# Performance work log

Measured on AMD Instinct MI355X. Metric: run time of the kernel, lower is better.

Reference implementation:

```python
import jax, jax.numpy as jnp
import numpy as np

B, S, H, NH = 4, 2048, 1024, 16
HD = H // NH
EPS = 1e-12


def setup_inputs() -> dict:
    key = jax.random.key(0)
    ks = jax.random.split(key, 12)
    sc = 0.02
    return {
        "query": jax.random.normal(ks[0], (B, S, H), dtype=jnp.float32),
        "attention_mask": jnp.zeros((B, 1, 1, S), dtype=jnp.float32),
        "Wq": jax.random.normal(ks[1], (H, H), dtype=jnp.float32) * sc,
        "bq": jnp.zeros((H,), dtype=jnp.float32),
        "Wk": jax.random.normal(ks[2], (H, H), dtype=jnp.float32) * sc,
        "bk": jnp.zeros((H,), dtype=jnp.float32),
        "Wv": jax.random.normal(ks[3], (H, H), dtype=jnp.float32) * sc,
        "bv": jnp.zeros((H,), dtype=jnp.float32),
        "Wd": jax.random.normal(ks[4], (H, H), dtype=jnp.float32) * sc,
        "bd": jnp.zeros((H,), dtype=jnp.float32),
        "ln_gamma": jnp.ones((H,), dtype=jnp.float32),
        "ln_beta": jnp.zeros((H,), dtype=jnp.float32),
    }


def reference(query, attention_mask, Wq, bq, Wk, bk, Wv, bv, Wd, bd, ln_gamma, ln_beta):
    # QKV projections: [B,S,H] -> [B,S,NH,HD]
    q = (query @ Wq + bq).reshape(B, S, NH, HD)
    k = (query @ Wk + bk).reshape(B, S, NH, HD)
    v = (query @ Wv + bv).reshape(B, S, NH, HD)
    # scores: [B,NH,S,S]
    scores = jnp.einsum("bqhd,bkhd->bhqk", q, k) / jnp.sqrt(jnp.float32(HD))
    scores = scores + attention_mask
    probs = jax.nn.softmax(scores, axis=-1)  # attn_dropout p=0 (eval)
    ctx = jnp.einsum("bhqk,bkhd->bqhd", probs, v).reshape(B, S, H)
    hidden = ctx @ Wd + bd  # out_dropout p=0 (eval)
    # pre-LN residual path: LN(hidden) + query
    mu = jnp.mean(hidden, axis=-1, keepdims=True)
    var = jnp.mean(jnp.square(hidden - mu), axis=-1, keepdims=True)
    hidden = (hidden - mu) * jax.lax.rsqrt(var + EPS) * ln_gamma + ln_beta
    return hidden + query
```

## Files before the change

### kernel.cpp

```cpp
#include <hip/hip_runtime.h>
#include <stdint.h>

#define Bn 4
#define Sn 2048
#define Hn 1024
#define NHn 16
#define Mn 8192

typedef unsigned short bf_t;
typedef __attribute__((ext_vector_type(8))) short s16x8;
typedef __attribute__((ext_vector_type(4))) short s16x4;
typedef __attribute__((ext_vector_type(8))) unsigned short u16x8;
typedef __attribute__((ext_vector_type(4))) unsigned short u16x4;
typedef __attribute__((ext_vector_type(4))) float f32x4;
typedef __attribute__((ext_vector_type(4))) unsigned int u32x4;
typedef __attribute__((ext_vector_type(2))) unsigned int u32x2;

__device__ __forceinline__ bf_t f2bf(float f) {
  unsigned int u = __float_as_uint(f);
  u += 0x7fffu + ((u >> 16) & 1u);
  return (bf_t)(u >> 16);
}

__device__ __forceinline__ unsigned pk2(float lo, float hi) {
  return __builtin_amdgcn_perm(__float_as_uint(hi), __float_as_uint(lo), 0x07060302u);
}
__device__ __forceinline__ s16x4 pack4(float a0, float a1, float a2, float a3) {
  u32x2 t;
  t[0] = pk2(a0, a1);
  t[1] = pk2(a2, a3);
  return __builtin_bit_cast(s16x4, t);
}

#define MFMA16K16(a, b, c) __builtin_amdgcn_mfma_f32_16x16x16bf16_1k(a, b, c, 0, 0, 0)
#define MFMA32(a, b, c) __builtin_amdgcn_mfma_f32_16x16x32_bf16(a, b, c, 0, 0, 0)

#define GLOAD16(gp, lp) __builtin_amdgcn_global_load_lds(              \
    (__attribute__((address_space(1))) void*)(gp),                     \
    (__attribute__((address_space(3))) void*)(lp), 16, 0, 0)

__global__ __launch_bounds__(256)
void prep(const float* __restrict__ Wq, const float* __restrict__ Wk,
          const float* __restrict__ Wv, const float* __restrict__ Wd,
          const float* __restrict__ query,
          bf_t* __restrict__ Wt, bf_t* __restrict__ Wdt, bf_t* __restrict__ Xb) {
  __shared__ float tile[32][33];
  const int z = blockIdx.z;
  const int tx = threadIdx.x;
  const int ty = threadIdx.y;
  if (z == 4) {
    const int bid = blockIdx.y * 32 + blockIdx.x;
    const int t = ty * 32 + tx;
    const size_t base = (size_t)bid * 8192 + t * 4;
#pragma unroll
    for (int i = 0; i < 8; i++) {
      const f32x4 v = *(const f32x4*)(query + base + i * 1024);
      u16x4 o;
      o[0] = f2bf(v[0]); o[1] = f2bf(v[1]); o[2] = f2bf(v[2]); o[3] = f2bf(v[3]);
      *(u16x4*)(Xb + base + i * 1024) = o;
    }
    return;
  }
  const float* W = (z == 0) ? Wq : (z == 1) ? Wk : (z == 2) ? Wv : Wd;
  bf_t* dst = (z < 3) ? Wt + (size_t)z * Hn * Hn : Wdt;
  const int n0 = blockIdx.x * 32, k0 = blockIdx.y * 32;
#pragma unroll
  for (int i = 0; i < 4; i++)
    tile[ty + i * 8][tx] = W[(size_t)(k0 + ty + i * 8) * Hn + n0 + tx];
  __syncthreads();
#pragma unroll
  for (int i = 0; i < 4; i++) {
    const int nn = ty + i * 8, kk = tx;
    dst[(size_t)(n0 + nn) * Hn + k0 + kk] = f2bf(tile[kk][nn]);
  }
}

__global__ __launch_bounds__(256, 3)
void gemm_bt(const bf_t* __restrict__ A, const bf_t* __restrict__ Bt,
             const float* __restrict__ b0, const float* __restrict__ b1,
             const float* __restrict__ b2, void* __restrict__ outp,
             int N, int K, int out_bf16)
{
  __shared__ bf_t As[2][4096];
  __shared__ bf_t Bs[2][4096];
  const int tid = threadIdx.x;
  const int wave = tid >> 6, lane = tid & 63;
  const int l15 = lane & 15, quad = lane >> 4;
  const int bm = blockIdx.y * 128, bn = blockIdx.x * 128;
  const int wm = (wave >> 1) * 64, wn = (wave & 1) * 64;
  const int srow = tid >> 2;
  const int scol = (tid & 3) * 8;

  const bf_t* Ag = A + (size_t)(bm + srow) * K + scol;
  const bf_t* Bg = Bt + (size_t)(bn + srow) * K + scol;

  f32x4 acc[4][4] = {};

  GLOAD16(Ag, As[0] + tid * 8);
  GLOAD16(Ag + (size_t)64 * K, As[0] + 2048 + tid * 8);
  GLOAD16(Bg, Bs[0] + tid * 8);
  GLOAD16(Bg + (size_t)64 * K, Bs[0] + 2048 + tid * 8);

  const int nIter = K >> 5;
  for (int i = 0; i < nIter; i++) {
    const int cur = i & 1;
    __syncthreads();
    if (i + 1 < nIter) {
      const int k0 = (i + 1) * 32;
      GLOAD16(Ag + k0, As[cur ^ 1] + tid * 8);
      GLOAD16(Ag + (size_t)64 * K + k0, As[cur ^ 1] + 2048 + tid * 8);
      GLOAD16(Bg + k0, Bs[cur ^ 1] + tid * 8);
      GLOAD16(Bg + (size_t)64 * K + k0, Bs[cur ^ 1] + 2048 + tid * 8);
    }
    s16x8 af[4], bfr[4];
#pragma unroll
    for (int mi = 0; mi < 4; mi++)
      af[mi] = *(const s16x8*)&As[cur][(wm + mi * 16 + l15) * 32 + quad * 8];
#pragma unroll
    for (int ni = 0; ni < 4; ni++)
      bfr[ni] = *(const s16x8*)&Bs[cur][(wn + ni * 16 + l15) * 32 + quad * 8];
#pragma unroll
    for (int mi = 0; mi < 4; mi++)
#pragma unroll
      for (int ni = 0; ni < 4; ni++)
        acc[mi][ni] = __builtin_amdgcn_mfma_f32_16x16x32_bf16(af[mi], bfr[ni], acc[mi][ni], 0, 0, 0);
  }

#pragma unroll
  for (int ni = 0; ni < 4; ni++) {
    const int gn = bn + wn + ni * 16 + l15;
    const float* bp = (gn < 1024) ? b0 : ((gn < 2048) ? b1 : b2);
    const float bias = bp[gn & 1023];
#pragma unroll
    for (int mi = 0; mi < 4; mi++) {
#pragma unroll
      for (int r = 0; r < 4; r++) {
        const int gm = bm + wm + mi * 16 + quad * 4 + r;
        const float v = acc[mi][ni][r] + bias;
        if (out_bf16) ((bf_t*)outp)[(size_t)gm * N + gn] = f2bf(v);
        else          ((float*)outp)[(size_t)gm * N + gn] = v;
      }
    }
  }
}

__global__ __launch_bounds__(256)
void kvswz(const bf_t* __restrict__ qkv, bf_t* __restrict__ Vf,
           const float* __restrict__ mask, bf_t* __restrict__ Fb) {
  __shared__ unsigned int P32[64 * 33];
  const int t = threadIdx.x;
  const int bh = blockIdx.y, b = bh >> 4, h = bh & 15;
  const int k0 = blockIdx.x * 64;

  {
    const int kp = t >> 3;
    const int d0 = (t & 7) * 8;
    const int kg = k0 + 2 * kp;
    const float f0 = __builtin_amdgcn_exp2f(mask[b * Sn + kg] * 1.44269504f);
    const float f1 = __builtin_amdgcn_exp2f(mask[b * Sn + kg + 1] * 1.44269504f);
    const bf_t* p0 = qkv + (size_t)(b * Sn + kg) * 3072 + 2048 + h * 64 + d0;
    const u16x8 r0 = *(const u16x8*)p0;
    const u16x8 r1 = *(const u16x8*)(p0 + 3072);
#pragma unroll
    for (int j = 0; j < 8; j++) {
      const float v0 = __uint_as_float((unsigned)r0[j] << 16) * f0;
      const float v1 = __uint_as_float((unsigned)r1[j] << 16) * f1;
      P32[(d0 + j) * 33 + kp] = pk2(v0, v1);
    }
  }
  if (h == 0 && t < 64) {
    const float fm = __builtin_amdgcn_exp2f(mask[b * Sn + k0 + t] * 1.44269504f);
    Fb[b * Sn + k0 + t] = f2bf(fm);
  }
  __syncthreads();
  bf_t* dst0 = Vf + ((size_t)(bh * 32 + blockIdx.x) * 8) * 512;
#pragma unroll
  for (int i = 0; i < 2; i++) {
    const int p = t + i * 256;
    const int fp = p >> 6, lane = p & 63;
    const int dvblk = fp >> 1, kpair = fp & 1;
    const int l15 = lane & 15, quad = (lane >> 4) & 3;
    const int d = dvblk * 16 + l15;
    const int c = kpair * 16 + quad * 2;
    u32x4 w;
    w[0] = P32[d * 33 + c];
    w[1] = P32[d * 33 + c + 1];
    w[2] = P32[d * 33 + c + 8];
    w[3] = P32[d * 33 + c + 9];
    *(u32x4*)(dst0 + (size_t)(kpair * 4 + dvblk) * 512 + lane * 8) = w;
  }
}

__global__ __launch_bounds__(512)
void attn(const bf_t* __restrict__ qkv, const bf_t* __restrict__ Vf,
          const bf_t* __restrict__ Fb, bf_t* __restrict__ ctx)
{
  __shared__ __align__(16) bf_t KV[2][2][2][2048];
  __shared__ __align__(16) bf_t Fs[2048];

  const int tid = threadIdx.x;
  const int wave = tid >> 6, lane = tid & 63;
  const int g = wave >> 2, wv = wave & 3;
  const int tg = tid & 255;
  const int l15 = lane & 15, quad = lane >> 4;
  const int idx = blockIdx.x;
  const int bh = idx & 63, b = bh >> 4, h = bh & 15;
  const int q0 = (idx >> 6) * 256;

  if (tid < 256) GLOAD16(Fb + (size_t)b * Sn + tid * 8, Fs + tid * 8);

  s16x8 aq[4][2];
#pragma unroll
  for (int qf = 0; qf < 4; qf++) {
    const bf_t* qp = qkv + (size_t)(b * Sn + q0 + wv * 64 + qf * 16 + l15) * 3072 + h * 64;
    aq[qf][0] = *(const s16x8*)(qp + quad * 8);
    aq[qf][1] = *(const s16x8*)(qp + 32 + quad * 8);
  }

  f32x4 lacc[4] = {};
  f32x4 o[4][4] = {};

  const int ks = tg >> 7, kh = (tg >> 6) & 1;
  const int lg = tg & 63, l15g = lg & 15, quadg = lg >> 4;
  const bf_t* kq = qkv + (size_t)(b * Sn + g * 1024 + ks * 16 + l15g) * 3072
                   + 1024 + h * 64 + kh * 32 + quadg * 8;
  const bf_t* vb = Vf + (size_t)bh * 131072 + (size_t)g * 65536;
  const float C1 = 0.125f * 1.44269504f;

  GLOAD16(kq, KV[g][0][0] + tg * 8);
  GLOAD16(vb + tg * 8, KV[g][1][0] + tg * 8);

  for (int it = 0; it < 32; ++it) {
    const int cur = it & 1;
    __syncthreads();
    if (it < 31) {
      GLOAD16(kq + (size_t)(it + 1) * 98304, KV[g][0][cur ^ 1] + tg * 8);
      GLOAD16(vb + (it + 1) * 2048 + tg * 8, KV[g][1][cur ^ 1] + tg * 8);
    }

    s16x4 pb[4][2];
#pragma unroll
    for (int e = 0; e < 2; e++) {
      const s16x8 k0f = *(const s16x8*)&KV[g][0][cur][(e * 2 + 0) * 512 + lane * 8];
      const s16x8 k1f = *(const s16x8*)&KV[g][0][cur][(e * 2 + 1) * 512 + lane * 8];
      const s16x4 ff = *(const s16x4*)&Fs[g * 1024 + it * 32 + e * 16 + quad * 4];
#pragma unroll
      for (int qf = 0; qf < 4; qf++) {
        f32x4 acc = {};
        __builtin_amdgcn_s_setprio(1);
        acc = MFMA32(k0f, aq[qf][0], acc);
        acc = MFMA32(k1f, aq[qf][1], acc);
        __builtin_amdgcn_s_setprio(0);
        const float p0 = __builtin_amdgcn_exp2f(acc[0] * C1);
        const float p1 = __builtin_amdgcn_exp2f(acc[1] * C1);
        const float p2 = __builtin_amdgcn_exp2f(acc[2] * C1);
        const float p3 = __builtin_amdgcn_exp2f(acc[3] * C1);
        pb[qf][e] = pack4(p0, p1, p2, p3);
        lacc[qf] = MFMA16K16(ff, pb[qf][e], lacc[qf]);
      }
    }

    __builtin_amdgcn_s_setprio(1);
#pragma unroll
    for (int dvblk = 0; dvblk < 4; dvblk++) {
      const s16x8 vv = *(const s16x8*)&KV[g][1][cur][dvblk * 512 + lane * 8];
      const s16x4 vlo = {vv[0], vv[1], vv[2], vv[3]};
      const s16x4 vhi = {vv[4], vv[5], vv[6], vv[7]};
#pragma unroll
      for (int qf = 0; qf < 4; qf++) {
        o[qf][dvblk] = MFMA16K16(vlo, pb[qf][0], o[qf][dvblk]);
        o[qf][dvblk] = MFMA16K16(vhi, pb[qf][1], o[qf][dvblk]);
      }
    }
    __builtin_amdgcn_s_setprio(0);
  }

  float* sm = (float*)&KV[0][0][0][0];
  float* sl = (float*)&Fs[0];
#pragma unroll
  for (int qh = 0; qh < 2; qh++) {
    __syncthreads();
    if (g == 1) {
#pragma unroll
      for (int lq = 0; lq < 2; lq++) {
        const int qf = qh * 2 + lq;
        const int rp = wv * 32 + lq * 16 + l15;
#pragma unroll
        for (int dvblk = 0; dvblk < 4; dvblk++) {
          const int col = (dvblk * 16 + quad * 4 + l15 * 4) & 63;
          *(f32x4*)&sm[rp * 64 + col] = o[qf][dvblk];
        }
        if (quad == 0) sl[rp] = lacc[qf][0];
      }
    }
    __syncthreads();
    if (g == 0) {
#pragma unroll
      for (int lq = 0; lq < 2; lq++) {
        const int qf = qh * 2 + lq;
        const int rp = wv * 32 + lq * 16 + l15;
        const float inv = 1.f / (lacc[qf][0] + sl[rp]);
        const size_t grow = (size_t)(b * Sn + q0 + wv * 64 + qf * 16 + l15);
#pragma unroll
        for (int dvblk = 0; dvblk < 4; dvblk++) {
          const int col = (dvblk * 16 + quad * 4 + l15 * 4) & 63;
          const f32x4 o2 = *(const f32x4*)&sm[rp * 64 + col];
          u16x4 ov;
#pragma unroll
          for (int r = 0; r < 4; r++) ov[r] = f2bf((o[qf][dvblk][r] + o2[r]) * inv);
          *(u16x4*)&ctx[grow * Hn + h * 64 + dvblk * 16 + quad * 4] = ov;
        }
      }
    }
  }
}

__global__ __launch_bounds__(256)
void ln_res(const float* __restrict__ hid, const float* __restrict__ query,
            const float* __restrict__ gamma, const float* __restrict__ beta,
            float* __restrict__ out)
{
  const int row = blockIdx.x, t = threadIdx.x;
  const f32x4 h = *(const f32x4*)(hid + (size_t)row * Hn + t * 4);
  float s = h[0] + h[1] + h[2] + h[3];
  float ss = h[0]*h[0] + h[1]*h[1] + h[2]*h[2] + h[3]*h[3];
#pragma unroll
  for (int m = 32; m; m >>= 1) { s += __shfl_xor(s, m); ss += __shfl_xor(ss, m); }
  __shared__ float red[8];
  if ((t & 63) == 0) { red[t >> 6] = s; red[4 + (t >> 6)] = ss; }
  __syncthreads();
  s = red[0] + red[1] + red[2] + red[3];
  ss = red[4] + red[5] + red[6] + red[7];
  const float mu = s * (1.f / Hn);
  const float rs = rsqrtf(ss * (1.f / Hn) - mu * mu + 1e-12f);
  const f32x4 q = *(const f32x4*)(query + (size_t)row * Hn + t * 4);
  const f32x4 g = *(const f32x4*)(gamma + t * 4);
  const f32x4 be = *(const f32x4*)(beta + t * 4);
  f32x4 o;
#pragma unroll
  for (int j = 0; j < 4; j++) o[j] = (h[j] - mu) * rs * g[j] + be[j] + q[j];
  *(f32x4*)(out + (size_t)row * Hn + t * 4) = o;
}

extern "C" void kernel_launch(void* const* d_in, const int* in_sizes, int n_in,
                              void* d_out, int out_size, void* d_ws, size_t ws_size,
                              hipStream_t stream) {
  const float* query = (const float*)d_in[0];
  const float* mask  = (const float*)d_in[1];
  const float* Wq = (const float*)d_in[2];
  const float* bq = (const float*)d_in[3];
  const float* Wk = (const float*)d_in[4];
  const float* bk = (const float*)d_in[5];
  const float* Wv = (const float*)d_in[6];
  const float* bv = (const float*)d_in[7];
  const float* Wd = (const float*)d_in[8];
  const float* bd = (const float*)d_in[9];
  const float* gamma = (const float*)d_in[10];
  const float* beta  = (const float*)d_in[11];

  char* w = (char*)d_ws;
  bf_t* Xb  = (bf_t*)w;  w += (size_t)Mn * Hn * 2;
  bf_t* Wt  = (bf_t*)w;  w += (size_t)3 * Hn * Hn * 2;
  bf_t* Wdt = (bf_t*)w;  w += (size_t)Hn * Hn * 2;
  bf_t* QKV = (bf_t*)w;  w += (size_t)Mn * 3 * Hn * 2;
  bf_t* Vf  = (bf_t*)w;  w += (size_t)64 * 32 * 4096 * 2;
  bf_t* Ctx = (bf_t*)w;  w += (size_t)Mn * Hn * 2;
  float* Hid = (float*)w;  w += (size_t)Mn * Hn * 4;
  bf_t* Fb = (bf_t*)w;

  prep<<<dim3(32, 32, 5), dim3(32, 8), 0, stream>>>(Wq, Wk, Wv, Wd, query, Wt, Wdt, Xb);
  gemm_bt<<<dim3(24, 64), 256, 0, stream>>>(Xb, Wt, bq, bk, bv, QKV, 3072, 1024, 1);
  kvswz<<<dim3(32, 64), 256, 0, stream>>>(QKV, Vf, mask, Fb);
  attn<<<512, 512, 0, stream>>>(QKV, Vf, Fb, Ctx);
  gemm_bt<<<dim3(8, 64), 256, 0, stream>>>(Ctx, Wdt, bd, bd, bd, Hid, 1024, 1024, 0);
  ln_res<<<Mn, 256, 0, stream>>>(Hid, query, gamma, beta, (float*)d_out);
}
```

Measured before the change: 357.0 us.

## Halve attention block size to 256 threads with 128 queries per block

The attention kernel now runs 1024 blocks of 256 threads, each covering 128 queries with 2 waves per key-split group instead of 4. Each thread issues twice as many K/V staging loads per iteration to fill the same shared tiles. The cross-group reduction epilogue collapses to a single pass, since the shared scratch now holds all rows. The intent is more blocks and better occupancy and tail balance across CUs, at the cost of loading each K/V tile for half as many queries.

```diff
diff --git a/kernel.cpp b/kernel.cpp
--- a/kernel.cpp
+++ b/kernel.cpp
@@ -191,7 +191,7 @@
   }
 }
 
-__global__ __launch_bounds__(512)
+__global__ __launch_bounds__(256)
 void attn(const bf_t* __restrict__ qkv, const bf_t* __restrict__ Vf,
           const bf_t* __restrict__ Fb, bf_t* __restrict__ ctx)
 {
@@ -200,14 +200,14 @@
 
   const int tid = threadIdx.x;
   const int wave = tid >> 6, lane = tid & 63;
-  const int g = wave >> 2, wv = wave & 3;
-  const int tg = tid & 255;
+  const int g = wave >> 1, wv = wave & 1;
+  const int tg = tid & 127;
   const int l15 = lane & 15, quad = lane >> 4;
   const int idx = blockIdx.x;
   const int bh = idx & 63, b = bh >> 4, h = bh & 15;
-  const int q0 = (idx >> 6) * 256;
-
-  if (tid < 256) GLOAD16(Fb + (size_t)b * Sn + tid * 8, Fs + tid * 8);
+  const int q0 = (idx >> 6) * 128;
+
+  GLOAD16(Fb + (size_t)b * Sn + tid * 8, Fs + tid * 8);
 
   s16x8 aq[4][2];
 #pragma unroll
@@ -220,22 +220,28 @@
   f32x4 lacc[4] = {};
   f32x4 o[4][4] = {};
 
-  const int ks = tg >> 7, kh = (tg >> 6) & 1;
-  const int lg = tg & 63, l15g = lg & 15, quadg = lg >> 4;
-  const bf_t* kq = qkv + (size_t)(b * Sn + g * 1024 + ks * 16 + l15g) * 3072
-                   + 1024 + h * 64 + kh * 32 + quadg * 8;
+  const int lane_s = tg & 63, l15s = lane_s & 15, quads = lane_s >> 4;
+  const int halfs = tg >> 6;
+  const bf_t* kq = qkv + (size_t)(b * Sn + g * 1024 + l15s) * 3072
+                   + 1024 + h * 64 + halfs * 32 + quads * 8;
   const bf_t* vb = Vf + (size_t)bh * 131072 + (size_t)g * 65536;
   const float C1 = 0.125f * 1.44269504f;
 
-  GLOAD16(kq, KV[g][0][0] + tg * 8);
-  GLOAD16(vb + tg * 8, KV[g][1][0] + tg * 8);
+  GLOAD16(kq,                KV[g][0][0] + tg * 8);
+  GLOAD16(kq + 16 * 3072,    KV[g][0][0] + 1024 + tg * 8);
+  GLOAD16(vb + tg * 8,        KV[g][1][0] + tg * 8);
+  GLOAD16(vb + 1024 + tg * 8, KV[g][1][0] + 1024 + tg * 8);
 
   for (int it = 0; it < 32; ++it) {
     const int cur = it & 1;
     __syncthreads();
     if (it < 31) {
-      GLOAD16(kq + (size_t)(it + 1) * 98304, KV[g][0][cur ^ 1] + tg * 8);
-      GLOAD16(vb + (it + 1) * 2048 + tg * 8, KV[g][1][cur ^ 1] + tg * 8);
+      const bf_t* kn = kq + (size_t)(it + 1) * 98304;
+      GLOAD16(kn,             KV[g][0][cur ^ 1] + tg * 8);
+      GLOAD16(kn + 16 * 3072, KV[g][0][cur ^ 1] + 1024 + tg * 8);
+      const bf_t* vn = vb + (size_t)(it + 1) * 2048;
+      GLOAD16(vn + tg * 8,        KV[g][1][cur ^ 1] + tg * 8);
+      GLOAD16(vn + 1024 + tg * 8, KV[g][1][cur ^ 1] + 1024 + tg * 8);
     }
 
     s16x4 pb[4][2];
@@ -275,41 +281,36 @@
     __builtin_amdgcn_s_setprio(0);
   }
 
+  __syncthreads();
   float* sm = (float*)&KV[0][0][0][0];
   float* sl = (float*)&Fs[0];
-#pragma unroll
-  for (int qh = 0; qh < 2; qh++) {
-    __syncthreads();
-    if (g == 1) {
-#pragma unroll
-      for (int lq = 0; lq < 2; lq++) {
-        const int qf = qh * 2 + lq;
-        const int rp = wv * 32 + lq * 16 + l15;
-#pragma unroll
-        for (int dvblk = 0; dvblk < 4; dvblk++) {
-          const int col = (dvblk * 16 + quad * 4 + l15 * 4) & 63;
-          *(f32x4*)&sm[rp * 64 + col] = o[qf][dvblk];
-        }
-        if (quad == 0) sl[rp] = lacc[qf][0];
-      }
-    }
-    __syncthreads();
-    if (g == 0) {
-#pragma unroll
-      for (int lq = 0; lq < 2; lq++) {
-        const int qf = qh * 2 + lq;
-        const int rp = wv * 32 + lq * 16 + l15;
-        const float inv = 1.f / (lacc[qf][0] + sl[rp]);
-        const size_t grow = (size_t)(b * Sn + q0 + wv * 64 + qf * 16 + l15);
-#pragma unroll
-        for (int dvblk = 0; dvblk < 4; dvblk++) {
-          const int col = (dvblk * 16 + quad * 4 + l15 * 4) & 63;
-          const f32x4 o2 = *(const f32x4*)&sm[rp * 64 + col];
-          u16x4 ov;
-#pragma unroll
-          for (int r = 0; r < 4; r++) ov[r] = f2bf((o[qf][dvblk][r] + o2[r]) * inv);
-          *(u16x4*)&ctx[grow * Hn + h * 64 + dvblk * 16 + quad * 4] = ov;
-        }
+  if (g == 1) {
+#pragma unroll
+    for (int qf = 0; qf < 4; qf++) {
+      const int rp = wv * 64 + qf * 16 + l15;
+#pragma unroll
+      for (int dvblk = 0; dvblk < 4; dvblk++) {
+        const int col = (dvblk * 16 + quad * 4 + l15 * 4) & 63;
+        *(f32x4*)&sm[rp * 64 + col] = o[qf][dvblk];
+      }
+      if (quad == 0) sl[rp] = lacc[qf][0];
+    }
+  }
+  __syncthreads();
+  if (g == 0) {
+#pragma unroll
+    for (int qf = 0; qf < 4; qf++) {
+      const int rp = wv * 64 + qf * 16 + l15;
+      const float inv = 1.f / (lacc[qf][0] + sl[rp]);
+      const size_t grow = (size_t)(b * Sn + q0 + rp);
+#pragma unroll
+      for (int dvblk = 0; dvblk < 4; dvblk++) {
+        const int col = (dvblk * 16 + quad * 4 + l15 * 4) & 63;
+        const f32x4 o2 = *(const f32x4*)&sm[rp * 64 + col];
+        u16x4 ov;
+#pragma unroll
+        for (int r = 0; r < 4; r++) ov[r] = f2bf((o[qf][dvblk][r] + o2[r]) * inv);
+        *(u16x4*)&ctx[grow * Hn + h * 64 + dvblk * 16 + quad * 4] = ov;
       }
     }
   }
@@ -371,7 +372,7 @@
   prep<<<dim3(32, 32, 5), dim3(32, 8), 0, stream>>>(Wq, Wk, Wv, Wd, query, Wt, Wdt, Xb);
   gemm_bt<<<dim3(24, 64), 256, 0, stream>>>(Xb, Wt, bq, bk, bv, QKV, 3072, 1024, 1);
   kvswz<<<dim3(32, 64), 256, 0, stream>>>(QKV, Vf, mask, Fb);
-  attn<<<512, 512, 0, stream>>>(QKV, Vf, Fb, Ctx);
+  attn<<<1024, 256, 0, stream>>>(QKV, Vf, Fb, Ctx);
   gemm_bt<<<dim3(8, 64), 256, 0, stream>>>(Ctx, Wdt, bd, bd, bd, Hid, 1024, 1024, 0);
   ln_res<<<Mn, 256, 0, stream>>>(Hid, query, gamma, beta, (float*)d_out);
 }
```

Result: no change. 359.0 us (+0.6%).
